# Optimization experiments

Hardware: AMD Instinct MI355X
Metric: run time of the kernel (lower is better)

Reference implementation:

```python
import jax, jax.numpy as jnp
import numpy as np

B, SQ, SK, H, NH = 2, 2048, 2048, 1024, 16
HD = H // NH  # 64


def setup_inputs() -> dict:
    key = jax.random.key(0)
    ks = jax.random.split(key, 12)
    s = 1.0 / np.sqrt(H)
    inp = {
        "query": jax.random.normal(ks[0], (B, SQ, H), jnp.float32),
        "key": jax.random.normal(ks[1], (B, SK, H), jnp.float32),
        "value": jax.random.normal(ks[2], (B, SK, H), jnp.float32),
        # lower-triangular causal mask [B, SQ, SK]; nonzero = attend
        "causal_mask": jnp.broadcast_to(
            jnp.tril(jnp.ones((SQ, SK), jnp.int32)), (B, SQ, SK)
        ),
        "Wq": jax.random.uniform(ks[3], (H, H), jnp.float32, -s, s),
        "bq": jnp.zeros((H,), jnp.float32),
        "Wk": jax.random.uniform(ks[4], (H, H), jnp.float32, -s, s),
        "bk": jnp.zeros((H,), jnp.float32),
        "Wv": jax.random.uniform(ks[5], (H, H), jnp.float32, -s, s),
        "bv": jnp.zeros((H,), jnp.float32),
        "Wo": jax.random.uniform(ks[6], (H, H), jnp.float32, -s, s),
        "bo": jnp.zeros((H,), jnp.float32),
        "ln_g": jnp.ones((H,), jnp.float32),
        "ln_b": jnp.zeros((H,), jnp.float32),
    }
    return inp


def _layer_norm(x, g, b, eps=1e-5):
    mu = jnp.mean(x, axis=-1, keepdims=True)
    var = jnp.var(x, axis=-1, keepdims=True)
    return (x - mu) * jax.lax.rsqrt(var + eps) * g + b


def reference(query, key, value, causal_mask, Wq, bq, Wk, bk, Wv, bv, Wo, bo, ln_g, ln_b):
    # projections (torch Linear: x @ W.T + b)
    q = (query @ Wq.T + bq).reshape(B, SQ, NH, HD)
    k = (key @ Wk.T + bk).reshape(B, SK, NH, HD)
    v = (value @ Wv.T + bv).reshape(B, SK, NH, HD)
    # scores [B, NH, SQ, SK]
    scores = jnp.einsum("bqhd,bkhd->bhqk", q, k) / np.sqrt(HD).astype(np.float32)
    scores = jnp.where(causal_mask[:, None, :, :] == 0, -jnp.inf, scores)
    attn = jax.nn.softmax(scores, axis=-1)
    # dropout is identity in eval mode
    out = jnp.einsum("bhqk,bkhd->bqhd", attn, v).reshape(B, SQ, H)
    out = out @ Wo.T + bo
    return _layer_norm(query + out, ln_g, ln_b)
```

## Files before the change

### kernel.cpp

```cpp
#include <hip/hip_runtime.h>
#include <hip/hip_bf16.h>

#define SQL 2048
#define SKL 2048
#define HH  1024
#define NHH 16
#define HDD 64
#define BB  2
#define MM  (BB*SQL)

typedef __attribute__((ext_vector_type(8))) short short8;
typedef __attribute__((ext_vector_type(4))) short short4v;
typedef __attribute__((ext_vector_type(4))) float f32x4;
typedef unsigned short u16;

__device__ inline u16 f2bf(float f) {
    unsigned int u = __float_as_uint(f);
    u += 0x7fffu + ((u >> 16) & 1u);
    return (u16)(u >> 16);
}

__device__ inline void gl_lds16(const void* g, void* l) {
    __builtin_amdgcn_global_load_lds(
        (const __attribute__((address_space(1))) unsigned int*)g,
        (__attribute__((address_space(3))) unsigned int*)l, 16, 0, 0);
}

__global__ __launch_bounds__(256) void cvt_all_kernel(
    const float* __restrict__ q, const float* __restrict__ k, const float* __restrict__ v,
    const float* __restrict__ wq, const float* __restrict__ wk,
    const float* __restrict__ wv, const float* __restrict__ wo,
    u16* __restrict__ xq, u16* __restrict__ xk, u16* __restrict__ xv,
    u16* __restrict__ wqb, u16* __restrict__ wkb, u16* __restrict__ wvb, u16* __restrict__ wob)
{
    int b = blockIdx.x;
    const float* src; u16* dst;
    if      (b < 4096)  { src = q;  dst = xq; }
    else if (b < 8192)  { src = k;  dst = xk;  b -= 4096; }
    else if (b < 12288) { src = v;  dst = xv;  b -= 8192; }
    else if (b < 13312) { src = wq; dst = wqb; b -= 12288; }
    else if (b < 14336) { src = wk; dst = wkb; b -= 13312; }
    else if (b < 15360) { src = wv; dst = wvb; b -= 14336; }
    else                { src = wo; dst = wob; b -= 15360; }
    int i = (b * 256 + threadIdx.x) * 4;
    float4 vv = *(const float4*)(src + i);
    ushort4 oo;
    oo.x = f2bf(vv.x); oo.y = f2bf(vv.y); oo.z = f2bf(vv.z); oo.w = f2bf(vv.w);
    *(ushort4*)(dst + i) = oo;
}

template<int MODE>
__global__ __launch_bounds__(256) void gemm_kernel(
    const u16* __restrict__ A0, const u16* __restrict__ A1,
    const u16* __restrict__ W0, const u16* __restrict__ W1,
    const float* __restrict__ bias0, const float* __restrict__ bias1,
    u16* __restrict__ o0, u16* __restrict__ o1,
    const float* __restrict__ resid, float* __restrict__ outf)
{
    const int z = blockIdx.z;
    const u16* A = (MODE == 0 && z == 1) ? A1 : A0;
    const u16* W = (MODE == 0 && z == 1) ? W1 : W0;
    const float* bias = (MODE == 0 && z == 1) ? bias1 : bias0;
    u16* outb = (MODE == 0 && z == 1) ? o1 : o0;
    const float scale = (MODE == 0 && z == 0) ? 0.125f * 1.4426950408889634f : 1.0f;

    __shared__ u16 lds_a[128 * 32];
    __shared__ u16 lds_b[128 * 32];

    const int t = threadIdx.x;
    const int lane = t & 63;
    const int quad = lane >> 4;
    const int lo = lane & 15;
    const int wv = t >> 6;
    const int wm = (wv >> 1) * 64, wn = (wv & 1) * 64;
    const int m0 = blockIdx.x * 128;
    const int n0 = blockIdx.y * 128;

    f32x4 acc[4][4];
#pragma unroll
    for (int i = 0; i < 4; i++)
#pragma unroll
        for (int j = 0; j < 4; j++) acc[i][j] = (f32x4){0.f, 0.f, 0.f, 0.f};

    const int sl0 = t, sl1 = 256 + t;
    const int r0 = sl0 >> 2, c0 = ((sl0 & 3) ^ ((r0 >> 1) & 3)) * 8;
    const int r1 = sl1 >> 2, c1 = ((sl1 & 3) ^ ((r1 >> 1) & 3)) * 8;

    for (int k0 = 0; k0 < HH; k0 += 32) {
        gl_lds16(A + (size_t)(m0 + r0) * HH + k0 + c0, &lds_a[sl0 * 8]);
        gl_lds16(A + (size_t)(m0 + r1) * HH + k0 + c1, &lds_a[sl1 * 8]);
        gl_lds16(W + (size_t)(n0 + r0) * HH + k0 + c0, &lds_b[sl0 * 8]);
        gl_lds16(W + (size_t)(n0 + r1) * HH + k0 + c1, &lds_b[sl1 * 8]);
        __syncthreads();
        short8 af[4], bf[4];
#pragma unroll
        for (int i = 0; i < 4; i++) {
            const int ra = wm + i * 16 + lo;
            const int rb = wn + i * 16 + lo;
            af[i] = *(const short8*)&lds_a[ra * 32 + ((quad ^ ((ra >> 1) & 3)) * 8)];
            bf[i] = *(const short8*)&lds_b[rb * 32 + ((quad ^ ((rb >> 1) & 3)) * 8)];
        }
#pragma unroll
        for (int i = 0; i < 4; i++)
#pragma unroll
            for (int j = 0; j < 4; j++) {
                if (MODE == 2)
                    acc[i][j] = __builtin_amdgcn_mfma_f32_16x16x32_bf16(bf[j], af[i], acc[i][j], 0, 0, 0);
                else
                    acc[i][j] = __builtin_amdgcn_mfma_f32_16x16x32_bf16(af[i], bf[j], acc[i][j], 0, 0, 0);
            }
        __syncthreads();
    }

#pragma unroll
    for (int i = 0; i < 4; i++) {
#pragma unroll
        for (int j = 0; j < 4; j++) {
#pragma unroll
            for (int r = 0; r < 4; r++) {
                if (MODE == 2) {
                    int dg  = n0 + wn + j * 16 + quad * 4 + r;
                    int tok = m0 + wm + i * 16 + lo;
                    float val = acc[i][j][r] + bias[dg];
                    int head = dg >> 6, d = dg & 63;
                    int bi = tok >> 11, s = tok & 2047;
                    outb[(((size_t)bi * NHH + head) * HDD + d) * SKL + s] = f2bf(val);
                } else {
                    int row = m0 + wm + i * 16 + quad * 4 + r;
                    int col = n0 + wn + j * 16 + lo;
                    float val = acc[i][j][r] + bias[col];
                    if (MODE == 0) {
                        val *= scale;
                        int bi = row >> 11, s = row & 2047;
                        int head = col >> 6, d = col & 63;
                        outb[(((size_t)bi * NHH + head) * SQL + s) * HDD + d] = f2bf(val);
                    } else {
                        val += resid[(size_t)row * HH + col];
                        outf[(size_t)row * HH + col] = val;
                    }
                }
            }
        }
    }
}

#define PSTR 72

__global__ __launch_bounds__(256) void attn_kernel(
    const u16* __restrict__ qb, const u16* __restrict__ kb, const u16* __restrict__ vtb,
    u16* __restrict__ attn_out)
{
    __shared__ u16 k_lds[64 * 64];
    __shared__ u16 vt_lds[64 * 64];
    __shared__ u16 p_lds[4 * 16 * PSTR];

    const int t = threadIdx.x;
    const int lane = t & 63;
    const int quad = lane >> 4;
    const int lo = lane & 15;
    const int w = t >> 6;
    const int qt = (SQL / 64 - 1) - (blockIdx.x >> 5);
    const int bh = blockIdx.x & 31;
    const int q0 = qt * 64;

    const u16* qbase = qb + ((size_t)bh * SQL + q0 + w * 16 + lo) * HDD + quad * 8;
    short8 qf0 = *(const short8*)qbase;
    short8 qf1 = *(const short8*)(qbase + 32);

    float m_s = -__builtin_inff(), l_s = 0.f;
    f32x4 o[4];
#pragma unroll
    for (int j = 0; j < 4; j++) o[j] = (f32x4){0.f, 0.f, 0.f, 0.f};

    const int sl0 = t, sl1 = 256 + t;
    const int r0 = sl0 >> 3, c0 = ((sl0 & 7) ^ (r0 & 7)) * 8;
    const int r1 = sl1 >> 3, c1 = ((sl1 & 7) ^ (r1 & 7)) * 8;
    const u16* kbh = kb + (size_t)bh * SKL * HDD;
    const u16* vbh = vtb + (size_t)bh * HDD * SKL;
    u16* ppriv = &p_lds[w * 16 * PSTR];

    for (int kt = 0; kt <= qt; kt++) {
        const int k0 = kt * 64;
        gl_lds16(kbh + (size_t)(k0 + r0) * HDD + c0, &k_lds[sl0 * 8]);
        gl_lds16(kbh + (size_t)(k0 + r1) * HDD + c1, &k_lds[sl1 * 8]);
        gl_lds16(vbh + (size_t)r0 * SKL + k0 + c0, &vt_lds[sl0 * 8]);
        gl_lds16(vbh + (size_t)r1 * SKL + k0 + c1, &vt_lds[sl1 * 8]);
        __syncthreads();

        f32x4 s[4];
#pragma unroll
        for (int nt = 0; nt < 4; nt++) {
            const int row = nt * 16 + lo;
            short8 kf0 = *(const short8*)&k_lds[row * 64 + ((quad ^ (row & 7)) * 8)];
            short8 kf1 = *(const short8*)&k_lds[row * 64 + (((4 + quad) ^ (row & 7)) * 8)];
            s[nt] = (f32x4){0.f, 0.f, 0.f, 0.f};
            s[nt] = __builtin_amdgcn_mfma_f32_16x16x32_bf16(kf0, qf0, s[nt], 0, 0, 0);
            s[nt] = __builtin_amdgcn_mfma_f32_16x16x32_bf16(kf1, qf1, s[nt], 0, 0, 0);
        }
        if (kt == qt) {
            const int ql = w * 16 + lo;
#pragma unroll
            for (int nt = 0; nt < 4; nt++)
#pragma unroll
                for (int r = 0; r < 4; r++)
                    if (nt * 16 + quad * 4 + r > ql) s[nt][r] = -__builtin_inff();
        }

        float mx = s[0][0];
#pragma unroll
        for (int nt = 0; nt < 4; nt++)
#pragma unroll
            for (int r = 0; r < 4; r++) mx = fmaxf(mx, s[nt][r]);
        mx = fmaxf(mx, __shfl_xor(mx, 16));
        mx = fmaxf(mx, __shfl_xor(mx, 32));
        float mnew = fmaxf(m_s, mx);
        float al = __builtin_amdgcn_exp2f(m_s - mnew);
        m_s = mnew;
        float rs = 0.f;
#pragma unroll
        for (int nt = 0; nt < 4; nt++)
#pragma unroll
            for (int r = 0; r < 4; r++) {
                s[nt][r] = __builtin_amdgcn_exp2f(s[nt][r] - m_s);
                rs += s[nt][r];
            }
        rs += __shfl_xor(rs, 16);
        rs += __shfl_xor(rs, 32);
        l_s = l_s * al + rs;

        float alr[4];
#pragma unroll
        for (int r = 0; r < 4; r++) alr[r] = __shfl(al, quad * 4 + r, 16);
#pragma unroll
        for (int nt = 0; nt < 4; nt++)
#pragma unroll
            for (int r = 0; r < 4; r++) o[nt][r] *= alr[r];

#pragma unroll
        for (int nt = 0; nt < 4; nt++) {
            short4v pk;
#pragma unroll
            for (int r = 0; r < 4; r++) pk[r] = (short)f2bf(s[nt][r]);
            *(short4v*)&ppriv[lo * PSTR + nt * 16 + quad * 4] = pk;
        }
        short8 pf0 = *(const short8*)&ppriv[lo * PSTR + quad * 8];
        short8 pf1 = *(const short8*)&ppriv[lo * PSTR + 32 + quad * 8];

#pragma unroll
        for (int nt = 0; nt < 4; nt++) {
            const int row = nt * 16 + lo;
            short8 vf0 = *(const short8*)&vt_lds[row * 64 + ((quad ^ (row & 7)) * 8)];
            short8 vf1 = *(const short8*)&vt_lds[row * 64 + (((4 + quad) ^ (row & 7)) * 8)];
            o[nt] = __builtin_amdgcn_mfma_f32_16x16x32_bf16(pf0, vf0, o[nt], 0, 0, 0);
            o[nt] = __builtin_amdgcn_mfma_f32_16x16x32_bf16(pf1, vf1, o[nt], 0, 0, 0);
        }
        __syncthreads();
    }

    const int b = bh >> 4, h = bh & 15;
    float inv[4];
#pragma unroll
    for (int r = 0; r < 4; r++) inv[r] = 1.0f / __shfl(l_s, quad * 4 + r, 16);
#pragma unroll
    for (int nt = 0; nt < 4; nt++)
#pragma unroll
        for (int r = 0; r < 4; r++) {
            int srow = q0 + w * 16 + quad * 4 + r;
            attn_out[((size_t)b * SQL + srow) * HH + h * HDD + nt * 16 + lo] =
                f2bf(o[nt][r] * inv[r]);
        }
}

__global__ __launch_bounds__(256) void ln_kernel(const float* __restrict__ x,
                                                 const float* __restrict__ g,
                                                 const float* __restrict__ bb,
                                                 float* __restrict__ out)
{
    const int row = blockIdx.x;
    const int t = threadIdx.x;
    const float* xr = x + (size_t)row * HH;
    float4 v = *(const float4*)(xr + t * 4);
    float s1 = v.x + v.y + v.z + v.w;
    float s2 = v.x * v.x + v.y * v.y + v.z * v.z + v.w * v.w;
#pragma unroll
    for (int off = 32; off; off >>= 1) { s1 += __shfl_xor(s1, off); s2 += __shfl_xor(s2, off); }
    __shared__ float red[8];
    if ((t & 63) == 0) { red[(t >> 6) * 2] = s1; red[(t >> 6) * 2 + 1] = s2; }
    __syncthreads();
    s1 = red[0] + red[2] + red[4] + red[6];
    s2 = red[1] + red[3] + red[5] + red[7];
    float mu = s1 * (1.0f / HH);
    float var = s2 * (1.0f / HH) - mu * mu;
    float rstd = rsqrtf(var + 1e-5f);
    float4 gg = *(const float4*)(g + t * 4);
    float4 b4 = *(const float4*)(bb + t * 4);
    float4 o;
    o.x = (v.x - mu) * rstd * gg.x + b4.x;
    o.y = (v.y - mu) * rstd * gg.y + b4.y;
    o.z = (v.z - mu) * rstd * gg.z + b4.z;
    o.w = (v.w - mu) * rstd * gg.w + b4.w;
    *(float4*)(out + (size_t)row * HH + t * 4) = o;
}

extern "C" void kernel_launch(void* const* d_in, const int* in_sizes, int n_in,
                              void* d_out, int out_size, void* d_ws, size_t ws_size,
                              hipStream_t stream)
{
    const float* query = (const float*)d_in[0];
    const float* key   = (const float*)d_in[1];
    const float* value = (const float*)d_in[2];
    const float* Wq = (const float*)d_in[4];
    const float* bq = (const float*)d_in[5];
    const float* Wk = (const float*)d_in[6];
    const float* bk = (const float*)d_in[7];
    const float* Wv = (const float*)d_in[8];
    const float* bv = (const float*)d_in[9];
    const float* Wo = (const float*)d_in[10];
    const float* bo = (const float*)d_in[11];
    const float* ln_g = (const float*)d_in[12];
    const float* ln_b = (const float*)d_in[13];
    float* out = (float*)d_out;

    char* wp = (char*)d_ws;
    auto alloc = [&](size_t bytes) { void* p = (void*)wp; wp += (bytes + 255) & ~(size_t)255; return p; };
    const int nW = HH * HH;
    const int nX = MM * HH;
    u16* wqb = (u16*)alloc((size_t)nW * 2);
    u16* wkb = (u16*)alloc((size_t)nW * 2);
    u16* wvb = (u16*)alloc((size_t)nW * 2);
    u16* wob = (u16*)alloc((size_t)nW * 2);
    u16* xq  = (u16*)alloc((size_t)nX * 2);
    u16* xk  = (u16*)alloc((size_t)nX * 2);
    u16* xv  = (u16*)alloc((size_t)nX * 2);
    u16* qbuf = (u16*)alloc((size_t)nX * 2);
    u16* kbuf = (u16*)alloc((size_t)nX * 2);
    u16* vbuf = (u16*)alloc((size_t)nX * 2);
    u16* attnb = (u16*)alloc((size_t)nX * 2);
    float* projf = (float*)alloc((size_t)nX * 4);

    cvt_all_kernel<<<16384, 256, 0, stream>>>(query, key, value, Wq, Wk, Wv, Wo,
                                              xq, xk, xv, wqb, wkb, wvb, wob);

    gemm_kernel<0><<<dim3(32, 8, 2), 256, 0, stream>>>(
        xq, xk, wqb, wkb, bq, bk, qbuf, kbuf, nullptr, nullptr);
    gemm_kernel<2><<<dim3(32, 8, 1), 256, 0, stream>>>(
        xv, xv, wvb, wvb, bv, bv, vbuf, vbuf, nullptr, nullptr);

    attn_kernel<<<1024, 256, 0, stream>>>(qbuf, kbuf, vbuf, attnb);

    gemm_kernel<1><<<dim3(32, 8, 1), 256, 0, stream>>>(
        attnb, attnb, wob, wob, bo, bo, nullptr, nullptr, query, projf);

    ln_kernel<<<MM, 256, 0, stream>>>(projf, ln_g, ln_b, out);
}
```

Before: 266.8 us.

## Fuse activation bf16 conversion into QKV GEMM and split-K the output projection

Activation fp32-to-bf16 conversion moves out of the standalone convert kernel and into the QKV GEMM's A-tile load path, and the three projections merge into one launch with z=3. This removes the write and re-read of the bf16 activation copies. The output projection is split along K into two halves written to separate fp32 buffers, and the LayerNorm kernel sums them, which doubles the grid for occupancy. In exchange, the A loads become synchronous register loads instead of direct global-to-LDS transfers, and the split-K path adds an extra fp32 buffer write and read.

```diff
diff --git a/kernel.cpp b/kernel.cpp
--- a/kernel.cpp
+++ b/kernel.cpp
@@ -26,22 +26,17 @@
         (__attribute__((address_space(3))) unsigned int*)l, 16, 0, 0);
 }
 
-__global__ __launch_bounds__(256) void cvt_all_kernel(
-    const float* __restrict__ q, const float* __restrict__ k, const float* __restrict__ v,
+__global__ __launch_bounds__(256) void cvt_w_kernel(
     const float* __restrict__ wq, const float* __restrict__ wk,
     const float* __restrict__ wv, const float* __restrict__ wo,
-    u16* __restrict__ xq, u16* __restrict__ xk, u16* __restrict__ xv,
     u16* __restrict__ wqb, u16* __restrict__ wkb, u16* __restrict__ wvb, u16* __restrict__ wob)
 {
     int b = blockIdx.x;
     const float* src; u16* dst;
-    if      (b < 4096)  { src = q;  dst = xq; }
-    else if (b < 8192)  { src = k;  dst = xk;  b -= 4096; }
-    else if (b < 12288) { src = v;  dst = xv;  b -= 8192; }
-    else if (b < 13312) { src = wq; dst = wqb; b -= 12288; }
-    else if (b < 14336) { src = wk; dst = wkb; b -= 13312; }
-    else if (b < 15360) { src = wv; dst = wvb; b -= 14336; }
-    else                { src = wo; dst = wob; b -= 15360; }
+    if      (b < 1024) { src = wq; dst = wqb; }
+    else if (b < 2048) { src = wk; dst = wkb; b -= 1024; }
+    else if (b < 3072) { src = wv; dst = wvb; b -= 2048; }
+    else               { src = wo; dst = wob; b -= 3072; }
     int i = (b * 256 + threadIdx.x) * 4;
     float4 vv = *(const float4*)(src + i);
     ushort4 oo;
@@ -49,20 +44,18 @@
     *(ushort4*)(dst + i) = oo;
 }
 
-template<int MODE>
-__global__ __launch_bounds__(256) void gemm_kernel(
-    const u16* __restrict__ A0, const u16* __restrict__ A1,
-    const u16* __restrict__ W0, const u16* __restrict__ W1,
-    const float* __restrict__ bias0, const float* __restrict__ bias1,
-    u16* __restrict__ o0, u16* __restrict__ o1,
-    const float* __restrict__ resid, float* __restrict__ outf)
+__global__ __launch_bounds__(256) void qkv_gemm_kernel(
+    const float* __restrict__ xq, const float* __restrict__ xk, const float* __restrict__ xv,
+    const u16* __restrict__ wqb, const u16* __restrict__ wkb, const u16* __restrict__ wvb,
+    const float* __restrict__ bq, const float* __restrict__ bk, const float* __restrict__ bv,
+    u16* __restrict__ oq, u16* __restrict__ ok, u16* __restrict__ ov)
 {
     const int z = blockIdx.z;
-    const u16* A = (MODE == 0 && z == 1) ? A1 : A0;
-    const u16* W = (MODE == 0 && z == 1) ? W1 : W0;
-    const float* bias = (MODE == 0 && z == 1) ? bias1 : bias0;
-    u16* outb = (MODE == 0 && z == 1) ? o1 : o0;
-    const float scale = (MODE == 0 && z == 0) ? 0.125f * 1.4426950408889634f : 1.0f;
+    const float* A = (z == 0) ? xq : (z == 1) ? xk : xv;
+    const u16* W = (z == 0) ? wqb : (z == 1) ? wkb : wvb;
+    const float* bias = (z == 0) ? bq : (z == 1) ? bk : bv;
+    u16* outb = (z == 0) ? oq : (z == 1) ? ok : ov;
+    const float scale = (z == 0) ? 0.125f * 1.4426950408889634f : 1.0f;
 
     __shared__ u16 lds_a[128 * 32];
     __shared__ u16 lds_b[128 * 32];
@@ -71,8 +64,8 @@
     const int lane = t & 63;
     const int quad = lane >> 4;
     const int lo = lane & 15;
-    const int wv = t >> 6;
-    const int wm = (wv >> 1) * 64, wn = (wv & 1) * 64;
+    const int wv_ = t >> 6;
+    const int wm = (wv_ >> 1) * 64, wn = (wv_ & 1) * 64;
     const int m0 = blockIdx.x * 128;
     const int n0 = blockIdx.y * 128;
 
@@ -85,10 +78,27 @@
     const int sl0 = t, sl1 = 256 + t;
     const int r0 = sl0 >> 2, c0 = ((sl0 & 3) ^ ((r0 >> 1) & 3)) * 8;
     const int r1 = sl1 >> 2, c1 = ((sl1 & 3) ^ ((r1 >> 1) & 3)) * 8;
+    const float* arow0 = A + (size_t)(m0 + r0) * HH + c0;
+    const float* arow1 = A + (size_t)(m0 + r1) * HH + c1;
 
     for (int k0 = 0; k0 < HH; k0 += 32) {
-        gl_lds16(A + (size_t)(m0 + r0) * HH + k0 + c0, &lds_a[sl0 * 8]);
-        gl_lds16(A + (size_t)(m0 + r1) * HH + k0 + c1, &lds_a[sl1 * 8]);
+        {
+            float4 f0 = *(const float4*)(arow0 + k0);
+            float4 f1 = *(const float4*)(arow0 + k0 + 4);
+            float4 f2 = *(const float4*)(arow1 + k0);
+            float4 f3 = *(const float4*)(arow1 + k0 + 4);
+            short8 h0, h1;
+            h0[0] = (short)f2bf(f0.x); h0[1] = (short)f2bf(f0.y);
+            h0[2] = (short)f2bf(f0.z); h0[3] = (short)f2bf(f0.w);
+            h0[4] = (short)f2bf(f1.x); h0[5] = (short)f2bf(f1.y);
+            h0[6] = (short)f2bf(f1.z); h0[7] = (short)f2bf(f1.w);
+            h1[0] = (short)f2bf(f2.x); h1[1] = (short)f2bf(f2.y);
+            h1[2] = (short)f2bf(f2.z); h1[3] = (short)f2bf(f2.w);
+            h1[4] = (short)f2bf(f3.x); h1[5] = (short)f2bf(f3.y);
+            h1[6] = (short)f2bf(f3.z); h1[7] = (short)f2bf(f3.w);
+            *(short8*)&lds_a[sl0 * 8] = h0;
+            *(short8*)&lds_a[sl1 * 8] = h1;
+        }
         gl_lds16(W + (size_t)(n0 + r0) * HH + k0 + c0, &lds_b[sl0 * 8]);
         gl_lds16(W + (size_t)(n0 + r1) * HH + k0 + c1, &lds_b[sl1 * 8]);
         __syncthreads();
@@ -100,15 +110,19 @@
             af[i] = *(const short8*)&lds_a[ra * 32 + ((quad ^ ((ra >> 1) & 3)) * 8)];
             bf[i] = *(const short8*)&lds_b[rb * 32 + ((quad ^ ((rb >> 1) & 3)) * 8)];
         }
-#pragma unroll
-        for (int i = 0; i < 4; i++)
-#pragma unroll
-            for (int j = 0; j < 4; j++) {
-                if (MODE == 2)
+        if (z == 2) {
+#pragma unroll
+            for (int i = 0; i < 4; i++)
+#pragma unroll
+                for (int j = 0; j < 4; j++)
                     acc[i][j] = __builtin_amdgcn_mfma_f32_16x16x32_bf16(bf[j], af[i], acc[i][j], 0, 0, 0);
-                else
+        } else {
+#pragma unroll
+            for (int i = 0; i < 4; i++)
+#pragma unroll
+                for (int j = 0; j < 4; j++)
                     acc[i][j] = __builtin_amdgcn_mfma_f32_16x16x32_bf16(af[i], bf[j], acc[i][j], 0, 0, 0);
-            }
+        }
         __syncthreads();
     }
 
@@ -118,7 +132,7 @@
         for (int j = 0; j < 4; j++) {
 #pragma unroll
             for (int r = 0; r < 4; r++) {
-                if (MODE == 2) {
+                if (z == 2) {
                     int dg  = n0 + wn + j * 16 + quad * 4 + r;
                     int tok = m0 + wm + i * 16 + lo;
                     float val = acc[i][j][r] + bias[dg];
@@ -128,17 +142,80 @@
                 } else {
                     int row = m0 + wm + i * 16 + quad * 4 + r;
                     int col = n0 + wn + j * 16 + lo;
-                    float val = acc[i][j][r] + bias[col];
-                    if (MODE == 0) {
-                        val *= scale;
-                        int bi = row >> 11, s = row & 2047;
-                        int head = col >> 6, d = col & 63;
-                        outb[(((size_t)bi * NHH + head) * SQL + s) * HDD + d] = f2bf(val);
-                    } else {
-                        val += resid[(size_t)row * HH + col];
-                        outf[(size_t)row * HH + col] = val;
-                    }
+                    float val = (acc[i][j][r] + bias[col]) * scale;
+                    int bi = row >> 11, s = row & 2047;
+                    int head = col >> 6, d = col & 63;
+                    outb[(((size_t)bi * NHH + head) * SQL + s) * HDD + d] = f2bf(val);
                 }
+            }
+        }
+    }
+}
+
+__global__ __launch_bounds__(256) void oproj_kernel(
+    const u16* __restrict__ A, const u16* __restrict__ W,
+    const float* __restrict__ bias, const float* __restrict__ resid,
+    float* __restrict__ p0, float* __restrict__ p1)
+{
+    const int z = blockIdx.z;
+    float* outf = z ? p1 : p0;
+
+    __shared__ u16 lds_a[128 * 32];
+    __shared__ u16 lds_b[128 * 32];
+
+    const int t = threadIdx.x;
+    const int lane = t & 63;
+    const int quad = lane >> 4;
+    const int lo = lane & 15;
+    const int wv_ = t >> 6;
+    const int wm = (wv_ >> 1) * 64, wn = (wv_ & 1) * 64;
+    const int m0 = blockIdx.x * 128;
+    const int n0 = blockIdx.y * 128;
+
+    f32x4 acc[4][4];
+#pragma unroll
+    for (int i = 0; i < 4; i++)
+#pragma unroll
+        for (int j = 0; j < 4; j++) acc[i][j] = (f32x4){0.f, 0.f, 0.f, 0.f};
+
+    const int sl0 = t, sl1 = 256 + t;
+    const int r0 = sl0 >> 2, c0 = ((sl0 & 3) ^ ((r0 >> 1) & 3)) * 8;
+    const int r1 = sl1 >> 2, c1 = ((sl1 & 3) ^ ((r1 >> 1) & 3)) * 8;
+
+    const int kbeg = z * 512, kend = kbeg + 512;
+    for (int k0 = kbeg; k0 < kend; k0 += 32) {
+        gl_lds16(A + (size_t)(m0 + r0) * HH + k0 + c0, &lds_a[sl0 * 8]);
+        gl_lds16(A + (size_t)(m0 + r1) * HH + k0 + c1, &lds_a[sl1 * 8]);
+        gl_lds16(W + (size_t)(n0 + r0) * HH + k0 + c0, &lds_b[sl0 * 8]);
+        gl_lds16(W + (size_t)(n0 + r1) * HH + k0 + c1, &lds_b[sl1 * 8]);
+        __syncthreads();
+        short8 af[4], bf[4];
+#pragma unroll
+        for (int i = 0; i < 4; i++) {
+            const int ra = wm + i * 16 + lo;
+            const int rb = wn + i * 16 + lo;
+            af[i] = *(const short8*)&lds_a[ra * 32 + ((quad ^ ((ra >> 1) & 3)) * 8)];
+            bf[i] = *(const short8*)&lds_b[rb * 32 + ((quad ^ ((rb >> 1) & 3)) * 8)];
+        }
+#pragma unroll
+        for (int i = 0; i < 4; i++)
+#pragma unroll
+            for (int j = 0; j < 4; j++)
+                acc[i][j] = __builtin_amdgcn_mfma_f32_16x16x32_bf16(af[i], bf[j], acc[i][j], 0, 0, 0);
+        __syncthreads();
+    }
+
+#pragma unroll
+    for (int i = 0; i < 4; i++) {
+#pragma unroll
+        for (int j = 0; j < 4; j++) {
+#pragma unroll
+            for (int r = 0; r < 4; r++) {
+                int row = m0 + wm + i * 16 + quad * 4 + r;
+                int col = n0 + wn + j * 16 + lo;
+                float val = acc[i][j][r];
+                if (z == 0) val += bias[col] + resid[(size_t)row * HH + col];
+                outf[(size_t)row * HH + col] = val;
             }
         }
     }
@@ -271,15 +348,18 @@
         }
 }
 
-__global__ __launch_bounds__(256) void ln_kernel(const float* __restrict__ x,
+__global__ __launch_bounds__(256) void ln_kernel(const float* __restrict__ p0,
+                                                 const float* __restrict__ p1,
                                                  const float* __restrict__ g,
                                                  const float* __restrict__ bb,
                                                  float* __restrict__ out)
 {
     const int row = blockIdx.x;
     const int t = threadIdx.x;
-    const float* xr = x + (size_t)row * HH;
-    float4 v = *(const float4*)(xr + t * 4);
+    float4 a = *(const float4*)(p0 + (size_t)row * HH + t * 4);
+    float4 c = *(const float4*)(p1 + (size_t)row * HH + t * 4);
+    float4 v;
+    v.x = a.x + c.x; v.y = a.y + c.y; v.z = a.z + c.z; v.w = a.w + c.w;
     float s1 = v.x + v.y + v.z + v.w;
     float s2 = v.x * v.x + v.y * v.y + v.z * v.z + v.w * v.w;
 #pragma unroll
@@ -329,27 +409,21 @@
     u16* wkb = (u16*)alloc((size_t)nW * 2);
     u16* wvb = (u16*)alloc((size_t)nW * 2);
     u16* wob = (u16*)alloc((size_t)nW * 2);
-    u16* xq  = (u16*)alloc((size_t)nX * 2);
-    u16* xk  = (u16*)alloc((size_t)nX * 2);
-    u16* xv  = (u16*)alloc((size_t)nX * 2);
     u16* qbuf = (u16*)alloc((size_t)nX * 2);
     u16* kbuf = (u16*)alloc((size_t)nX * 2);
     u16* vbuf = (u16*)alloc((size_t)nX * 2);
     u16* attnb = (u16*)alloc((size_t)nX * 2);
-    float* projf = (float*)alloc((size_t)nX * 4);
-
-    cvt_all_kernel<<<16384, 256, 0, stream>>>(query, key, value, Wq, Wk, Wv, Wo,
-                                              xq, xk, xv, wqb, wkb, wvb, wob);
-
-    gemm_kernel<0><<<dim3(32, 8, 2), 256, 0, stream>>>(
-        xq, xk, wqb, wkb, bq, bk, qbuf, kbuf, nullptr, nullptr);
-    gemm_kernel<2><<<dim3(32, 8, 1), 256, 0, stream>>>(
-        xv, xv, wvb, wvb, bv, bv, vbuf, vbuf, nullptr, nullptr);
+    float* p0 = (float*)alloc((size_t)nX * 4);
+    float* p1 = (float*)alloc((size_t)nX * 4);
+
+    cvt_w_kernel<<<4096, 256, 0, stream>>>(Wq, Wk, Wv, Wo, wqb, wkb, wvb, wob);
+
+    qkv_gemm_kernel<<<dim3(32, 8, 3), 256, 0, stream>>>(
+        query, key, value, wqb, wkb, wvb, bq, bk, bv, qbuf, kbuf, vbuf);
 
     attn_kernel<<<1024, 256, 0, stream>>>(qbuf, kbuf, vbuf, attnb);
 
-    gemm_kernel<1><<<dim3(32, 8, 1), 256, 0, stream>>>(
-        attnb, attnb, wob, wob, bo, bo, nullptr, nullptr, query, projf);
-
-    ln_kernel<<<MM, 256, 0, stream>>>(projf, ln_g, ln_b, out);
-}
+    oproj_kernel<<<dim3(32, 8, 2), 256, 0, stream>>>(attnb, wob, bo, query, p0, p1);
+
+    ln_kernel<<<MM, 256, 0, stream>>>(p0, p1, ln_g, ln_b, out);
+}
```

Result: slower. 322.3 us (+20.8%).
